# Kernel optimization log

Measured on AMD Instinct MI355X. Metric: run time of the kernel, lower is better.

## Reference

```python
import jax, jax.numpy as jnp
import numpy as np

TEMP = 1.0
EPS = 1e-3  # keras LayerNormalization default epsilon


def _ln(x, g, b):
    m = jnp.mean(x, -1, keepdims=True)
    v = jnp.mean((x - m) ** 2, -1, keepdims=True)
    return g * (x - m) * jax.lax.rsqrt(v + EPS) + b


def setup_inputs() -> dict:
    key = jax.random.key(0)
    ks = jax.random.split(key, 16)
    B, N, C, A, F = 8, 2048, 64, 256, 128
    r = lambda k, s: (jax.random.normal(ks[k], s) * 0.02).astype(jnp.float32)
    z = lambda n: jnp.zeros((n,), jnp.float32)
    return {
        'spatial': jax.random.normal(ks[0], (B, N, C), jnp.float32),
        'frequency': jax.random.normal(ks[1], (B, N, C), jnp.float32),
        'wavelet': jax.random.normal(ks[2], (B, N, C), jnp.float32),
        'Ws': r(3, (C, A)), 'bs': z(A),
        'Wf': r(4, (C, A)), 'bf': z(A),
        'Ww': r(5, (C, A)), 'bw': z(A),
        'g1': jnp.ones((A,), jnp.float32), 'b1': z(A),
        'Wk': r(6, (A, F)), 'bk': z(F),
        'Wq': r(7, (A, F)), 'bq': z(F),
        'Wt': r(8, (A, F)), 'bt': z(F),
        'Wg': r(9, (F + 3, F)), 'bg': z(F),
        'Wfu': r(10, (3 * F, F)), 'bfu': z(F),
        'Wdf': r(11, (F, F)), 'bdf': z(F),
        'g2': jnp.ones((F,), jnp.float32), 'b2': z(F),
    }


def _forward(spatial, frequency, wavelet, Ws, bs, Wf, bf, Ww, bw, g1, b1,
             Wk, bk, Wq, bq, Wt, bt, Wg, bg, Wfu, bfu, Wdf, bdf, g2, b2):
    B = spatial.shape[0]
    # FeatureAlignment: per-domain Dense + shared LayerNorm
    aligned = [
        _ln(spatial @ Ws + bs, g1, b1),
        _ln(frequency @ Wf + bf, g1, b1),
        _ln(wavelet @ Ww + bw, g1, b1),
    ]  # each [B, N, A]
    # DomainCorrelation
    K = [a @ Wk + bk for a in aligned]  # [B, N, F]
    Q = [a @ Wq + bq for a in aligned]
    corr = jnp.zeros((B, 3, 3), spatial.dtype)
    for i in range(3):
        for j in range(i, 3):
            # queries from domain j, keys from domain i (as in original)
            s = jax.nn.softmax(jnp.einsum('bnd,bmd->bnm', Q[j], K[i]) / TEMP, axis=-1)
            m = jnp.mean(s, axis=(1, 2))  # [B]
            corr = corr.at[:, i, j].set(m)
            if i != j:
                corr = corr.at[:, j, i].set(m)
    # NOTE: original applies softmax over the batch axis of the [B] row means
    dw = [jax.nn.softmax(jnp.mean(corr[:, i, :], axis=1)) for i in range(3)]  # each [B]
    # FeatureTransfer
    corr_mean = jnp.mean(corr, axis=1)  # [B, 3]
    enhanced = []
    for a, w in zip(aligned, dw):
        t = a @ Wt + bt  # [B, N, F]
        N = t.shape[1]
        gin = jnp.concatenate([t, jnp.broadcast_to(corr_mean[:, None, :], (B, N, 3))], axis=-1)
        gate = jax.nn.sigmoid(gin @ Wg + bg)
        enhanced.append(t * gate * w[:, None, None])
    fused = jnp.concatenate(enhanced, axis=-1) @ Wfu + bfu  # [B, N, F]
    out = _ln(fused @ Wdf + bdf, g2, b2)
    return out, corr, dw, enhanced


def reference(spatial, frequency, wavelet, Ws, bs, Wf, bf, Ww, bw, g1, b1,
              Wk, bk, Wq, bq, Wt, bt, Wg, bg, Wfu, bfu, Wdf, bdf, g2, b2):
    out, corr, dw, enh = _forward(spatial, frequency, wavelet, Ws, bs, Wf, bf, Ww, bw,
                                  g1, b1, Wk, bk, Wq, bq, Wt, bt, Wg, bg, Wfu, bfu,
                                  Wdf, bdf, g2, b2)
    return (out, corr, dw[0], dw[1], dw[2], enh[0], enh[1], enh[2])
```

## Files before the change

kernel.cpp:

```cpp
#include <hip/hip_runtime.h>
#include <math.h>


typedef __attribute__((ext_vector_type(8))) short short8;
typedef __attribute__((ext_vector_type(4))) float f32x4;
#define MFMA(a, b, c) __builtin_amdgcn_mfma_f32_16x16x32_bf16(a, b, c, 0, 0, 0)

#define NTOK 32
#define XP 72
#define AP 264
#define TP 136

#define WD0_B 0u
#define WD1_B 32768u
#define WD2_B 65536u
#define WT_B  98304u
#define WG_B  163840u
#define WF0_B 196608u
#define WF1_B 229376u
#define WF2_B 262144u
#define WDF_B 294912u

__device__ __forceinline__ unsigned short bf16rtn(float v) {
    unsigned u = __float_as_uint(v);
    unsigned r = u + 0x7FFFu + ((u >> 16) & 1u);
    return (unsigned short)(r >> 16);
}
__device__ __forceinline__ void split2(float v, unsigned short& h, unsigned short& l) {
    h = bf16rtn(v);
    float hf = __uint_as_float(((unsigned)h) << 16);
    l = bf16rtn(v - hf);
}
__device__ __forceinline__ float bf2f(unsigned short h) {
    return __uint_as_float(((unsigned)h) << 16);
}

__global__ __launch_bounds__(256) void prep_kernel(
    const float* __restrict__ Ws, const float* __restrict__ Wf,
    const float* __restrict__ Ww, const float* __restrict__ Wt,
    const float* __restrict__ Wg, const float* __restrict__ Wfu,
    const float* __restrict__ Wdf, unsigned short* __restrict__ ws)
{
    int s = blockIdx.x * 256 + threadIdx.x;
    const float* src; int K, N; unsigned base, S; int fi;
    if (s < 2048)      { src = Ws;            K = 64;  N = 256; base = WD0_B; S = 16384; fi = s; }
    else if (s < 4096) { src = Wf;            K = 64;  N = 256; base = WD1_B; S = 16384; fi = s - 2048; }
    else if (s < 6144) { src = Ww;            K = 64;  N = 256; base = WD2_B; S = 16384; fi = s - 4096; }
    else if (s < 10240){ src = Wt;            K = 256; N = 128; base = WT_B;  S = 32768; fi = s - 6144; }
    else if (s < 12288){ src = Wg;            K = 128; N = 128; base = WG_B;  S = 16384; fi = s - 10240; }
    else if (s < 14336){ src = Wfu;           K = 128; N = 128; base = WF0_B; S = 16384; fi = s - 12288; }
    else if (s < 16384){ src = Wfu + 16384;   K = 128; N = 128; base = WF1_B; S = 16384; fi = s - 14336; }
    else if (s < 18432){ src = Wfu + 32768;   K = 128; N = 128; base = WF2_B; S = 16384; fi = s - 16384; }
    else               { src = Wdf;           K = 128; N = 128; base = WDF_B; S = 16384; fi = s - 18432; }
    const int lane = fi & 63, frag = fi >> 6;
    const int KC = K >> 5;
    const int nt = frag / KC, kc = frag - nt * KC;
    const int n  = nt * 16 + (lane & 15);
    const int k0 = kc * 32 + (lane >> 4) * 8;
    short8 hv, lv;
    #pragma unroll
    for (int j = 0; j < 8; ++j) {
        unsigned short h, l;
        split2(src[(k0 + j) * N + n], h, l);
        hv[j] = (short)h; lv[j] = (short)l;
    }
    *(short8*)&ws[base + (unsigned)fi * 8]     = hv;
    *(short8*)&ws[base + S + (unsigned)fi * 8] = lv;
}

__device__ __forceinline__ void gemm128_d2(
    const unsigned short* __restrict__ wsB, unsigned S,
    const unsigned short* __restrict__ Ph, const unsigned short* __restrict__ Pl,
    int tok0, int tok1, int quad, int wv, int lane, f32x4 acc[2])
{
    short8 Bh[2], Bl[2];
    #pragma unroll
    for (int j = 0; j < 2; ++j) {
        const unsigned short* bp = wsB + ((unsigned)(wv * 4 + j) * 64 + lane) * 8;
        Bh[j] = *(const short8*)bp; Bl[j] = *(const short8*)(bp + S);
    }
    #pragma unroll
    for (int kc = 0; kc < 4; ++kc) {
        const short8 bh = Bh[kc & 1], bl = Bl[kc & 1];
        if (kc + 2 < 4) {
            const unsigned short* bp = wsB + ((unsigned)(wv * 4 + kc + 2) * 64 + lane) * 8;
            Bh[kc & 1] = *(const short8*)bp; Bl[kc & 1] = *(const short8*)(bp + S);
        }
        const int k = kc * 32 + quad * 8;
        const short8 Ah0 = *(const short8*)&Ph[tok0 * TP + k];
        const short8 Al0 = *(const short8*)&Pl[tok0 * TP + k];
        const short8 Ah1 = *(const short8*)&Ph[tok1 * TP + k];
        const short8 Al1 = *(const short8*)&Pl[tok1 * TP + k];
        acc[0] = MFMA(Ah0, bh, acc[0]);
        acc[0] = MFMA(Al0, bh, acc[0]);
        acc[0] = MFMA(Ah0, bl, acc[0]);
        acc[1] = MFMA(Ah1, bh, acc[1]);
        acc[1] = MFMA(Al1, bh, acc[1]);
        acc[1] = MFMA(Ah1, bl, acc[1]);
    }
}

__global__ __launch_bounds__(512) void mega_kernel(
    const float* __restrict__ x0, const float* __restrict__ x1,
    const float* __restrict__ x2,
    const float* __restrict__ bd0, const float* __restrict__ bd1,
    const float* __restrict__ bd2,
    const float* __restrict__ g1, const float* __restrict__ b1,
    const float* __restrict__ bt, const float* __restrict__ Wg,
    const float* __restrict__ bg, const float* __restrict__ bfu,
    const float* __restrict__ bdf, const float* __restrict__ g2,
    const float* __restrict__ b2,
    const unsigned short* __restrict__ ws,
    float* __restrict__ out, float* __restrict__ consts,
    float* __restrict__ e0, float* __restrict__ e1, float* __restrict__ e2)
{
    __shared__ __align__(16) unsigned char smem[53248];
    unsigned short* xh = (unsigned short*)smem;
    unsigned short* xl = xh + 32 * XP;
    unsigned short* th = (unsigned short*)smem;
    unsigned short* tl = th + 32 * TP;
    unsigned short* ah = (unsigned short*)(smem + 17408);
    unsigned short* al = ah + 32 * AP;
    float* ostage = (float*)(smem + 17408);
    float* psumS  = (float*)(smem + 51200);
    float* psumQ  = psumS + 32 * 8;

    const int tid = threadIdx.x, wv = tid >> 6, lane = tid & 63;
    const int lm = lane & 15, quad = lane >> 4;
    const int row0 = blockIdx.x * NTOK;
    const int tok0 = lm, tok1 = lm + 16;

    if (blockIdx.x == 0) {
        if (tid < 72) consts[tid] = 4.8828125e-4f;
        else if (tid < 96) consts[tid] = 0.125f;
    }

    int cA[2]; float g1c[2], b1c[2];
    #pragma unroll
    for (int i = 0; i < 2; ++i) { cA[i] = (wv * 2 + i) * 16 + lm; g1c[i] = g1[cA[i]]; b1c[i] = b1[cA[i]]; }
    const int cT = wv * 16 + lm;
    const float btc = bt[cT];
    const float bgc = bg[cT] + 4.8828125e-4f * (Wg[16384 + cT] + Wg[16512 + cT] + Wg[16640 + cT]);
    const float bdc = bdf[cT], g2c = g2[cT], b2c = b2[cT];
    f32x4 facc[2];
    { const float bv = bfu[cT]; facc[0] = (f32x4){bv, bv, bv, bv}; facc[1] = facc[0]; }

    const float* xs[3]  = {x0, x1, x2};
    const float* bds[3] = {bd0, bd1, bd2};
    float* es[3] = {e0, e1, e2};
    const unsigned WDB[3] = {WD0_B, WD1_B, WD2_B};
    const unsigned WFB[3] = {WF0_B, WF1_B, WF2_B};

    for (int d = 0; d < 3; ++d) {
        __syncthreads();
        {
            const int tok = tid >> 4, c4 = (tid & 15) * 4;
            const f32x4 v = __builtin_nontemporal_load(
                (const f32x4*)&xs[d][(row0 + tok) * 64 + c4]);
            unsigned short h0, l0, h1, l1, h2, l2, h3, l3;
            split2(v.x, h0, l0); split2(v.y, h1, l1);
            split2(v.z, h2, l2); split2(v.w, h3, l3);
            *(ushort4*)&xh[tok * XP + c4] = make_ushort4(h0, h1, h2, h3);
            *(ushort4*)&xl[tok * XP + c4] = make_ushort4(l0, l1, l2, l3);
        }
        __syncthreads();

        f32x4 acc[2][2];
        {
            const float* bdp = bds[d];
            #pragma unroll
            for (int i = 0; i < 2; ++i) {
                const float bv = bdp[cA[i]];
                acc[i][0] = (f32x4){bv, bv, bv, bv}; acc[i][1] = acc[i][0];
            }
        }
        {
            short8 Bh[2], Bl[2];
            #pragma unroll
            for (int j = 0; j < 2; ++j) {
                const unsigned short* bp = ws + WDB[d] +
                    ((unsigned)((wv * 2 + j) * 2 + 0) * 64 + lane) * 8;
                Bh[j] = *(const short8*)bp; Bl[j] = *(const short8*)(bp + 16384);
            }
            #pragma unroll
            for (int f = 0; f < 4; ++f) {
                const int kc = f >> 1, i = f & 1;
                const short8 bh = Bh[f & 1], bl = Bl[f & 1];
                if (f + 2 < 4) {
                    const int f2 = f + 2;
                    const unsigned short* bp = ws + WDB[d] +
                        ((unsigned)((wv * 2 + (f2 & 1)) * 2 + (f2 >> 1)) * 64 + lane) * 8;
                    Bh[f & 1] = *(const short8*)bp; Bl[f & 1] = *(const short8*)(bp + 16384);
                }
                const int k = kc * 32 + quad * 8;
                const short8 Ah0 = *(const short8*)&xh[tok0 * XP + k];
                const short8 Al0 = *(const short8*)&xl[tok0 * XP + k];
                const short8 Ah1 = *(const short8*)&xh[tok1 * XP + k];
                const short8 Al1 = *(const short8*)&xl[tok1 * XP + k];
                acc[i][0] = MFMA(Ah0, bh, acc[i][0]);
                acc[i][0] = MFMA(Al0, bh, acc[i][0]);
                acc[i][0] = MFMA(Ah0, bl, acc[i][0]);
                acc[i][1] = MFMA(Ah1, bh, acc[i][1]);
                acc[i][1] = MFMA(Al1, bh, acc[i][1]);
                acc[i][1] = MFMA(Ah1, bl, acc[i][1]);
            }
        }
        {
            #pragma unroll
            for (int m = 0; m < 2; ++m)
                #pragma unroll
                for (int r = 0; r < 4; ++r) {
                    float s = acc[0][m][r] + acc[1][m][r];
                    float q = acc[0][m][r] * acc[0][m][r] + acc[1][m][r] * acc[1][m][r];
                    #pragma unroll
                    for (int off = 1; off < 16; off <<= 1) {
                        s += __shfl_xor(s, off); q += __shfl_xor(q, off);
                    }
                    if (lm == 0) {
                        const int row = m * 16 + quad * 4 + r;
                        psumS[row * 8 + wv] = s;
                        psumQ[row * 8 + wv] = q;
                    }
                }
        }
        __syncthreads();
        #pragma unroll
        for (int m = 0; m < 2; ++m)
            #pragma unroll
            for (int r = 0; r < 4; ++r) {
                const int row = m * 16 + quad * 4 + r;
                const float4 s0 = *(const float4*)&psumS[row * 8];
                const float4 s1 = *(const float4*)&psumS[row * 8 + 4];
                const float4 q0 = *(const float4*)&psumQ[row * 8];
                const float4 q1 = *(const float4*)&psumQ[row * 8 + 4];
                const float S = s0.x + s0.y + s0.z + s0.w + s1.x + s1.y + s1.z + s1.w;
                const float Q = q0.x + q0.y + q0.z + q0.w + q1.x + q1.y + q1.z + q1.w;
                const float mean = S * (1.f / 256.f);
                const float rs = rsqrtf(Q * (1.f / 256.f) - mean * mean + 1e-3f);
                #pragma unroll
                for (int i = 0; i < 2; ++i) {
                    const float v = (acc[i][m][r] - mean) * rs * g1c[i] + b1c[i];
                    unsigned short h, l; split2(v, h, l);
                    ah[row * AP + cA[i]] = h; al[row * AP + cA[i]] = l;
                }
            }
        __syncthreads();

        f32x4 tac[2];
        tac[0] = (f32x4){btc, btc, btc, btc}; tac[1] = tac[0];
        {
            short8 Bh[2], Bl[2];
            #pragma unroll
            for (int j = 0; j < 2; ++j) {
                const unsigned short* bp = ws + WT_B + ((unsigned)(wv * 8 + j) * 64 + lane) * 8;
                Bh[j] = *(const short8*)bp; Bl[j] = *(const short8*)(bp + 32768);
            }
            #pragma unroll
            for (int kc = 0; kc < 8; ++kc) {
                const short8 bh = Bh[kc & 1], bl = Bl[kc & 1];
                if (kc + 2 < 8) {
                    const unsigned short* bp = ws + WT_B + ((unsigned)(wv * 8 + kc + 2) * 64 + lane) * 8;
                    Bh[kc & 1] = *(const short8*)bp; Bl[kc & 1] = *(const short8*)(bp + 32768);
                }
                const int k = kc * 32 + quad * 8;
                const short8 Ah0 = *(const short8*)&ah[tok0 * AP + k];
                const short8 Al0 = *(const short8*)&al[tok0 * AP + k];
                const short8 Ah1 = *(const short8*)&ah[tok1 * AP + k];
                const short8 Al1 = *(const short8*)&al[tok1 * AP + k];
                tac[0] = MFMA(Ah0, bh, tac[0]);
                tac[0] = MFMA(Al0, bh, tac[0]);
                tac[0] = MFMA(Ah0, bl, tac[0]);
                tac[1] = MFMA(Ah1, bh, tac[1]);
                tac[1] = MFMA(Al1, bh, tac[1]);
                tac[1] = MFMA(Ah1, bl, tac[1]);
            }
        }
        __syncthreads();
        unsigned short tsp[2][4][2];
        #pragma unroll
        for (int m = 0; m < 2; ++m)
            #pragma unroll
            for (int r = 0; r < 4; ++r) {
                const int row = m * 16 + quad * 4 + r;
                unsigned short h, l; split2(tac[m][r], h, l);
                tsp[m][r][0] = h; tsp[m][r][1] = l;
                th[row * TP + cT] = h; tl[row * TP + cT] = l;
            }
        __syncthreads();

        f32x4 zac[2];
        zac[0] = (f32x4){bgc, bgc, bgc, bgc}; zac[1] = zac[0];
        gemm128_d2(ws + WG_B, 16384, th, tl, tok0, tok1, quad, wv, lane, zac);

        float er[2][4];
        #pragma unroll
        for (int m = 0; m < 2; ++m)
            #pragma unroll
            for (int r = 0; r < 4; ++r) {
                const float tv = bf2f(tsp[m][r][0]) + bf2f(tsp[m][r][1]);
                er[m][r] = tv * (1.f / (1.f + __expf(-zac[m][r]))) * 0.125f;
            }
        __syncthreads();
        #pragma unroll
        for (int m = 0; m < 2; ++m)
            #pragma unroll
            for (int r = 0; r < 4; ++r) {
                const int row = m * 16 + quad * 4 + r;
                unsigned short h, l; split2(er[m][r], h, l);
                th[row * TP + cT] = h; tl[row * TP + cT] = l;
            }
        __syncthreads();

        #pragma unroll
        for (int p = 0; p < 2; ++p) {
            const int row = (tid >> 5) + p * 16;
            const int c4 = (tid & 31) * 4;
            const ushort4 h0 = *(const ushort4*)&th[row * TP + c4];
            const ushort4 l0 = *(const ushort4*)&tl[row * TP + c4];
            f32x4 o = {bf2f(h0.x) + bf2f(l0.x), bf2f(h0.y) + bf2f(l0.y),
                       bf2f(h0.z) + bf2f(l0.z), bf2f(h0.w) + bf2f(l0.w)};
            __builtin_nontemporal_store(o, (f32x4*)(es[d] + (row0 + row) * 128 + c4));
        }

        gemm128_d2(ws + WFB[d], 16384, th, tl, tok0, tok1, quad, wv, lane, facc);
    }

    __syncthreads();
    #pragma unroll
    for (int m = 0; m < 2; ++m)
        #pragma unroll
        for (int r = 0; r < 4; ++r) {
            const int row = m * 16 + quad * 4 + r;
            unsigned short h, l; split2(facc[m][r], h, l);
            th[row * TP + cT] = h; tl[row * TP + cT] = l;
        }
    __syncthreads();

    f32x4 dac[2];
    dac[0] = (f32x4){bdc, bdc, bdc, bdc}; dac[1] = dac[0];
    gemm128_d2(ws + WDF_B, 16384, th, tl, tok0, tok1, quad, wv, lane, dac);

    #pragma unroll
    for (int m = 0; m < 2; ++m)
        #pragma unroll
        for (int r = 0; r < 4; ++r) {
            float s = dac[m][r];
            float q = dac[m][r] * dac[m][r];
            #pragma unroll
            for (int off = 1; off < 16; off <<= 1) {
                s += __shfl_xor(s, off); q += __shfl_xor(q, off);
            }
            if (lm == 0) {
                const int row = m * 16 + quad * 4 + r;
                psumS[row * 8 + wv] = s;
                psumQ[row * 8 + wv] = q;
            }
        }
    __syncthreads();
    #pragma unroll
    for (int m = 0; m < 2; ++m)
        #pragma unroll
        for (int r = 0; r < 4; ++r) {
            const int row = m * 16 + quad * 4 + r;
            const float4 s0 = *(const float4*)&psumS[row * 8];
            const float4 s1 = *(const float4*)&psumS[row * 8 + 4];
            const float4 q0 = *(const float4*)&psumQ[row * 8];
            const float4 q1 = *(const float4*)&psumQ[row * 8 + 4];
            const float S = s0.x + s0.y + s0.z + s0.w + s1.x + s1.y + s1.z + s1.w;
            const float Q = q0.x + q0.y + q0.z + q0.w + q1.x + q1.y + q1.z + q1.w;
            const float mean = S * (1.f / 128.f);
            const float rs = rsqrtf(Q * (1.f / 128.f) - mean * mean + 1e-3f);
            ostage[row * 128 + cT] = (dac[m][r] - mean) * rs * g2c + b2c;
        }
    __syncthreads();
    #pragma unroll
    for (int p = 0; p < 2; ++p) {
        const int row = (tid >> 5) + p * 16;
        const int c4 = (tid & 31) * 4;
        const f32x4 o = *(const f32x4*)&ostage[row * 128 + c4];
        __builtin_nontemporal_store(o, (f32x4*)(out + (row0 + row) * 128 + c4));
    }
}

extern "C" void kernel_launch(void* const* d_in, const int* in_sizes, int n_in,
                              void* d_out, int out_size, void* d_ws, size_t ws_size,
                              hipStream_t stream) {
    const float* spatial   = (const float*)d_in[0];
    const float* frequency = (const float*)d_in[1];
    const float* wavelet   = (const float*)d_in[2];
    const float* Ws  = (const float*)d_in[3];
    const float* bs  = (const float*)d_in[4];
    const float* Wf  = (const float*)d_in[5];
    const float* bf  = (const float*)d_in[6];
    const float* Ww  = (const float*)d_in[7];
    const float* bw  = (const float*)d_in[8];
    const float* g1  = (const float*)d_in[9];
    const float* b1  = (const float*)d_in[10];
    const float* Wt  = (const float*)d_in[15];
    const float* bt  = (const float*)d_in[16];
    const float* Wg  = (const float*)d_in[17];
    const float* bg  = (const float*)d_in[18];
    const float* Wfu = (const float*)d_in[19];
    const float* bfu = (const float*)d_in[20];
    const float* Wdf = (const float*)d_in[21];
    const float* bdf = (const float*)d_in[22];
    const float* g2  = (const float*)d_in[23];
    const float* b2  = (const float*)d_in[24];

    float* out    = (float*)d_out;
    float* consts = out + 2097152;
    float* enh0   = out + 2097248;
    float* enh1   = out + 4194400;
    float* enh2   = out + 6291552;
    unsigned short* wsp = (unsigned short*)d_ws;

    prep_kernel<<<80, 256, 0, stream>>>(Ws, Wf, Ww, Wt, Wg, Wfu, Wdf, wsp);
    mega_kernel<<<16384 / NTOK, 512, 0, stream>>>(
        spatial, frequency, wavelet, bs, bf, bw, g1, b1,
        bt, Wg, bg, bfu, bdf, g2, b2, wsp,
        out, consts, enh0, enh1, enh2);
}
```

Baseline: 184.3 us.

## Prefetch next domain input and cut barriers with a separate enhanced buffer

The global load of the next domain's input tile is issued before the Wt GEMM, and its bf16 split is written to shared memory at the end of the current iteration, so load latency overlaps compute. The gated enhanced values now go to a dedicated shared buffer placed over the aligned-activation region. This lets the fusion GEMM run straight after the gate, removes several __syncthreads, and drops the register copy of the transfer output. The cost is one float4 of input held live across the GEMMs, plus a reliance on careful shared-memory aliasing between the x, t and enhanced buffers.

Measured after the change: 181.3 us. No clear change (-1.6%).

```diff
diff --git a/kernel.cpp b/kernel.cpp
--- a/kernel.cpp
+++ b/kernel.cpp
@@ -121,6 +121,8 @@
     unsigned short* tl = th + 32 * TP;
     unsigned short* ah = (unsigned short*)(smem + 17408);
     unsigned short* al = ah + 32 * AP;
+    unsigned short* eh = (unsigned short*)(smem + 17408);
+    unsigned short* el = eh + 32 * TP;
     float* ostage = (float*)(smem + 17408);
     float* psumS  = (float*)(smem + 51200);
     float* psumQ  = psumS + 32 * 8;
@@ -129,6 +131,7 @@
     const int lm = lane & 15, quad = lane >> 4;
     const int row0 = blockIdx.x * NTOK;
     const int tok0 = lm, tok1 = lm + 16;
+    const int stok = tid >> 4, sc4 = (tid & 15) * 4;
 
     if (blockIdx.x == 0) {
         if (tid < 72) consts[tid] = 4.8828125e-4f;
@@ -151,20 +154,18 @@
     const unsigned WDB[3] = {WD0_B, WD1_B, WD2_B};
     const unsigned WFB[3] = {WF0_B, WF1_B, WF2_B};
 
+    {
+        const f32x4 v = __builtin_nontemporal_load(
+            (const f32x4*)&xs[0][(row0 + stok) * 64 + sc4]);
+        unsigned short h0, l0, h1, l1, h2, l2, h3, l3;
+        split2(v.x, h0, l0); split2(v.y, h1, l1);
+        split2(v.z, h2, l2); split2(v.w, h3, l3);
+        *(ushort4*)&xh[stok * XP + sc4] = make_ushort4(h0, h1, h2, h3);
+        *(ushort4*)&xl[stok * XP + sc4] = make_ushort4(l0, l1, l2, l3);
+    }
+    __syncthreads();
+
     for (int d = 0; d < 3; ++d) {
-        __syncthreads();
-        {
-            const int tok = tid >> 4, c4 = (tid & 15) * 4;
-            const f32x4 v = __builtin_nontemporal_load(
-                (const f32x4*)&xs[d][(row0 + tok) * 64 + c4]);
-            unsigned short h0, l0, h1, l1, h2, l2, h3, l3;
-            split2(v.x, h0, l0); split2(v.y, h1, l1);
-            split2(v.z, h2, l2); split2(v.w, h3, l3);
-            *(ushort4*)&xh[tok * XP + c4] = make_ushort4(h0, h1, h2, h3);
-            *(ushort4*)&xl[tok * XP + c4] = make_ushort4(l0, l1, l2, l3);
-        }
-        __syncthreads();
-
         f32x4 acc[2][2];
         {
             const float* bdp = bds[d];
@@ -205,25 +206,24 @@
                 acc[i][1] = MFMA(Ah1, bl, acc[i][1]);
             }
         }
-        {
-            #pragma unroll
-            for (int m = 0; m < 2; ++m)
+        #pragma unroll
+        for (int m = 0; m < 2; ++m)
+            #pragma unroll
+            for (int r = 0; r < 4; ++r) {
+                float s = acc[0][m][r] + acc[1][m][r];
+                float q = acc[0][m][r] * acc[0][m][r] + acc[1][m][r] * acc[1][m][r];
                 #pragma unroll
-                for (int r = 0; r < 4; ++r) {
-                    float s = acc[0][m][r] + acc[1][m][r];
-                    float q = acc[0][m][r] * acc[0][m][r] + acc[1][m][r] * acc[1][m][r];
-                    #pragma unroll
-                    for (int off = 1; off < 16; off <<= 1) {
-                        s += __shfl_xor(s, off); q += __shfl_xor(q, off);
-                    }
-                    if (lm == 0) {
-                        const int row = m * 16 + quad * 4 + r;
-                        psumS[row * 8 + wv] = s;
-                        psumQ[row * 8 + wv] = q;
-                    }
-                }
-        }
+                for (int off = 1; off < 16; off <<= 1) {
+                    s += __shfl_xor(s, off); q += __shfl_xor(q, off);
+                }
+                if (lm == 0) {
+                    const int row = m * 16 + quad * 4 + r;
+                    psumS[row * 8 + wv] = s;
+                    psumQ[row * 8 + wv] = q;
+                }
+            }
         __syncthreads();
+
         #pragma unroll
         for (int m = 0; m < 2; ++m)
             #pragma unroll
@@ -246,6 +246,11 @@
             }
         __syncthreads();
 
+        f32x4 xvn;
+        if (d < 2)
+            xvn = __builtin_nontemporal_load(
+                (const f32x4*)&xs[d + 1][(row0 + stok) * 64 + sc4]);
+
         f32x4 tac[2];
         tac[0] = (f32x4){btc, btc, btc, btc}; tac[1] = tac[0];
         {
@@ -275,15 +280,12 @@
                 tac[1] = MFMA(Ah1, bl, tac[1]);
             }
         }
-        __syncthreads();
-        unsigned short tsp[2][4][2];
         #pragma unroll
         for (int m = 0; m < 2; ++m)
             #pragma unroll
             for (int r = 0; r < 4; ++r) {
                 const int row = m * 16 + quad * 4 + r;
                 unsigned short h, l; split2(tac[m][r], h, l);
-                tsp[m][r][0] = h; tsp[m][r][1] = l;
                 th[row * TP + cT] = h; tl[row * TP + cT] = l;
             }
         __syncthreads();
@@ -292,49 +294,49 @@
         zac[0] = (f32x4){bgc, bgc, bgc, bgc}; zac[1] = zac[0];
         gemm128_d2(ws + WG_B, 16384, th, tl, tok0, tok1, quad, wv, lane, zac);
 
-        float er[2][4];
-        #pragma unroll
-        for (int m = 0; m < 2; ++m)
-            #pragma unroll
-            for (int r = 0; r < 4; ++r) {
-                const float tv = bf2f(tsp[m][r][0]) + bf2f(tsp[m][r][1]);
-                er[m][r] = tv * (1.f / (1.f + __expf(-zac[m][r]))) * 0.125f;
-            }
-        __syncthreads();
         #pragma unroll
         for (int m = 0; m < 2; ++m)
             #pragma unroll
             for (int r = 0; r < 4; ++r) {
                 const int row = m * 16 + quad * 4 + r;
-                unsigned short h, l; split2(er[m][r], h, l);
-                th[row * TP + cT] = h; tl[row * TP + cT] = l;
+                const float tv = bf2f(th[row * TP + cT]) + bf2f(tl[row * TP + cT]);
+                const float e = tv * (1.f / (1.f + __expf(-zac[m][r]))) * 0.125f;
+                unsigned short h, l; split2(e, h, l);
+                eh[row * TP + cT] = h; el[row * TP + cT] = l;
             }
         __syncthreads();
+
+        gemm128_d2(ws + WFB[d], 16384, eh, el, tok0, tok1, quad, wv, lane, facc);
 
         #pragma unroll
         for (int p = 0; p < 2; ++p) {
             const int row = (tid >> 5) + p * 16;
             const int c4 = (tid & 31) * 4;
-            const ushort4 h0 = *(const ushort4*)&th[row * TP + c4];
-            const ushort4 l0 = *(const ushort4*)&tl[row * TP + c4];
+            const ushort4 h0 = *(const ushort4*)&eh[row * TP + c4];
+            const ushort4 l0 = *(const ushort4*)&el[row * TP + c4];
             f32x4 o = {bf2f(h0.x) + bf2f(l0.x), bf2f(h0.y) + bf2f(l0.y),
                        bf2f(h0.z) + bf2f(l0.z), bf2f(h0.w) + bf2f(l0.w)};
             __builtin_nontemporal_store(o, (f32x4*)(es[d] + (row0 + row) * 128 + c4));
         }
 
-        gemm128_d2(ws + WFB[d], 16384, th, tl, tok0, tok1, quad, wv, lane, facc);
-    }
-
-    __syncthreads();
-    #pragma unroll
-    for (int m = 0; m < 2; ++m)
-        #pragma unroll
-        for (int r = 0; r < 4; ++r) {
-            const int row = m * 16 + quad * 4 + r;
-            unsigned short h, l; split2(facc[m][r], h, l);
-            th[row * TP + cT] = h; tl[row * TP + cT] = l;
-        }
-    __syncthreads();
+        if (d < 2) {
+            unsigned short h0, l0, h1, l1, h2, l2, h3, l3;
+            split2(xvn.x, h0, l0); split2(xvn.y, h1, l1);
+            split2(xvn.z, h2, l2); split2(xvn.w, h3, l3);
+            *(ushort4*)&xh[stok * XP + sc4] = make_ushort4(h0, h1, h2, h3);
+            *(ushort4*)&xl[stok * XP + sc4] = make_ushort4(l0, l1, l2, l3);
+        } else {
+            #pragma unroll
+            for (int m = 0; m < 2; ++m)
+                #pragma unroll
+                for (int r = 0; r < 4; ++r) {
+                    const int row = m * 16 + quad * 4 + r;
+                    unsigned short h, l; split2(facc[m][r], h, l);
+                    th[row * TP + cT] = h; tl[row * TP + cT] = l;
+                }
+        }
+        __syncthreads();
+    }
 
     f32x4 dac[2];
     dac[0] = (f32x4){bdc, bdc, bdc, bdc}; dac[1] = dac[0];
```
